# Kernel optimization log

Measured on AMD Instinct MI355X. Metric: run time of the kernel, lower is better.

Reference implementation:

```python
import jax, jax.numpy as jnp
import numpy as np

N_NODES = 25000
N_EDGES = 320000
IN_FEAT = 64
OUT_FEAT = 64
NUM_HEADS = 5
NUM_RELS = 20
NUM_BASES = 10


def setup_inputs() -> dict:
    key = jax.random.key(0)
    ks = jax.random.split(key, 8)
    feat = jax.random.normal(ks[0], (N_NODES, IN_FEAT), dtype=jnp.float32)
    src = jax.random.randint(ks[1], (N_EDGES,), 0, N_NODES, dtype=jnp.int64 if jax.config.jax_enable_x64 else jnp.int32)
    dst = jax.random.randint(ks[2], (N_EDGES,), 0, N_NODES, dtype=src.dtype)
    edge_type = jax.random.randint(ks[3], (N_EDGES,), 0, NUM_RELS, dtype=src.dtype)
    fc_w = jax.random.normal(ks[4], (IN_FEAT, OUT_FEAT), dtype=jnp.float32) * (2.0 / np.sqrt(IN_FEAT + OUT_FEAT))
    self_fc_w = jax.random.normal(ks[5], (IN_FEAT, NUM_HEADS * OUT_FEAT), dtype=jnp.float32) * (2.0 / np.sqrt(IN_FEAT + NUM_HEADS * OUT_FEAT))
    attention_weight = jax.random.normal(ks[6], (NUM_BASES, 2 * OUT_FEAT, NUM_HEADS), dtype=jnp.float32) * (2.0 / np.sqrt(2 * OUT_FEAT + NUM_HEADS))
    w_comp = jax.random.normal(ks[7], (NUM_RELS, NUM_BASES), dtype=jnp.float32) * (2.0 / np.sqrt(NUM_RELS + NUM_BASES))
    return {"feat": feat, "src": src, "dst": dst, "edge_type": edge_type,
            "fc_w": fc_w, "self_fc_w": self_fc_w,
            "attention_weight": attention_weight, "w_comp": w_comp}


def reference(feat, src, dst, edge_type, fc_w, self_fc_w, attention_weight, w_comp):
    # node projections
    z = feat @ fc_w                      # [N, F]
    self_z = feat @ self_fc_w            # [N, H*F]
    # basis-composed per-relation attention matrices: [R, 2F, H]
    attn_fcs = jnp.einsum('rb,bfh->rfh', w_comp, attention_weight)
    # per-edge attention: cat(src_z, dst_z) bmm gathered relation matrix
    z2 = jnp.concatenate([z[src], z[dst]], axis=1)          # [E, 2F]
    w_e = attn_fcs[edge_type]                                # [E, 2F, H] irregular gather
    att = jax.nn.leaky_relu(jnp.einsum('ef,efh->eh', z2, w_e), negative_slope=0.01)  # [E, H]
    # message = outer(att, src_z) flattened, segment-summed over dst
    msg = (att[:, :, None] * z[src][:, None, :]).reshape(att.shape[0], -1)  # [E, H*F]
    h = jax.ops.segment_sum(msg, dst, num_segments=feat.shape[0])            # [N, H*F]
    h = h + self_z  # self interaction; activation is None
    return h
```

## Files before the change

### kernel.cpp

```cpp
#include <hip/hip_runtime.h>
#include <hip/hip_bf16.h>

#define N_NODES 25000
#define N_EDGES 320000
#define F 64
#define H 5
#define R 20
#define B 10
#define HF 320
#define GEMMB 391
#define SCATB 625
#define MPAD 25024
#define CAP 64

typedef __attribute__((ext_vector_type(8))) short short8;
typedef __attribute__((ext_vector_type(4))) short short4v;
typedef __attribute__((ext_vector_type(4))) float float4v;

__device__ __forceinline__ float ldf(const void* p, int f32, int i) {
    if (f32) return ((const float*)p)[i];
    else     return __bfloat162float(((const __hip_bfloat16*)p)[i]);
}
__device__ __forceinline__ int ldi(const void* p, int i64, int i) {
    if (i64) return ((const int*)p)[2 * i];
    else     return ((const int*)p)[i];
}
__device__ __forceinline__ float b2f(unsigned short u) {
    union { unsigned u32; float f; } v; v.u32 = ((unsigned)u) << 16; return v.f;
}
__device__ __forceinline__ short f2bs(float x) {
    __hip_bfloat16 v = __float2bfloat16(x); return *(short*)&v;
}

__device__ __forceinline__ int probe_f32(const void* feat_raw) {
    unsigned w = ((const unsigned*)feat_raw)[threadIdx.x & 63];
    unsigned e = (w >> 7) & 0xFF;
    unsigned long long m = __ballot(e >= 110 && e <= 140);
    return __popcll(m) < 32;
}
__device__ __forceinline__ int probe_i64(const void* src_raw) {
    unsigned v = ((const unsigned*)src_raw)[2 * (threadIdx.x & 63) + 1];
    unsigned long long m = __ballot(v == 0);
    return __popcll(m) > 32;
}

__global__ void k0_setup(const void* __restrict__ feat,
                         const void* __restrict__ fcw, const void* __restrict__ sfw,
                         const void* __restrict__ aw, const void* __restrict__ wc,
                         __hip_bfloat16* __restrict__ Wpack,
                         __hip_bfloat16* __restrict__ W2pack,
                         int* __restrict__ cnt) {
    const int f32 = probe_f32(feat);
    const int idx = blockIdx.x * 256 + threadIdx.x;
    if (idx < N_NODES) cnt[idx] = 0;
    if (idx < 24576) {
        int j = idx & 7, lane = (idx >> 3) & 63, fq = idx >> 9;
        int q = fq & 1, t = fq >> 1;
        int k = (q ? 32 : 0) + ((lane >> 4) << 3) + j;
        int c = t * 16 + (lane & 15);
        float v = (c < HF) ? ldf(sfw, f32, k * HF + c) : ldf(fcw, f32, k * F + (c - HF));
        Wpack[idx] = __float2bfloat16(v);
    } else if (idx < 24576 + 20480) {
        int id2 = idx - 24576;
        int j = id2 & 7, lane = (id2 >> 3) & 63, fq = id2 >> 9;
        int q = fq & 1, t = fq >> 1;
        int k = (q ? 32 : 0) + ((lane >> 4) << 3) + j;
        int c = t * 16 + (lane & 15);
        int r = c >> 4, part = (c >> 3) & 1, h = c & 7;
        float acc = 0.f;
        if (h < H) {
#pragma unroll
            for (int bb = 0; bb < B; ++bb)
                acc += ldf(wc, f32, r * B + bb) *
                       ldf(aw, f32, bb * (2 * F * H) + (part * F + k) * H + h);
        }
        W2pack[id2] = __float2bfloat16(acc);
    }
}

__global__ __launch_bounds__(512) void k2_gemm(const void* __restrict__ feat,
                                               const void* __restrict__ srcp,
                                               const void* __restrict__ dstp,
                                               const void* __restrict__ etp,
                                               const __hip_bfloat16* __restrict__ Wpack,
                                               const __hip_bfloat16* __restrict__ W2pack,
                                               __hip_bfloat16* __restrict__ selfz,
                                               __hip_bfloat16* __restrict__ zc,
                                               __hip_bfloat16* __restrict__ a_src,
                                               __hip_bfloat16* __restrict__ a_dst,
                                               int* __restrict__ cnt,
                                               unsigned* __restrict__ perm) {
    __shared__ short zl[64][66];
    const int tid = threadIdx.x;

    if (blockIdx.x >= GEMMB) {
        const int i64 = probe_i64(srcp);
        const int e = (blockIdx.x - GEMMB) * 512 + tid;
        if (e < N_EDGES) {
            int d = ldi(dstp, i64, e);
            int s = ldi(srcp, i64, e);
            int r = ldi(etp, i64, e);
            int pos = atomicAdd(&cnt[d], 1);
            if (pos < CAP) perm[d * CAP + pos] = ((unsigned)r << 16) | (unsigned)s;
        }
        return;
    }

    const int f32 = probe_f32(feat);
    const int wave = tid >> 6, lane = tid & 63;
    const int quad = lane >> 4, col = lane & 15;
    const int wv = wave & 3, gh = wave >> 2;
    const int r0 = blockIdx.x * 64;

    short8 a0g[2], a1g[2];
#pragma unroll
    for (int gg = 0; gg < 2; ++gg) {
        const int g = gh * 2 + gg;
        int am = r0 + g * 16 + col;
        if (am >= N_NODES) am = N_NODES - 1;
        if (f32) {
            const float* Af = (const float*)feat;
            float4v f0 = *(const float4v*)(Af + am * F + quad * 8);
            float4v f1 = *(const float4v*)(Af + am * F + quad * 8 + 4);
            float4v g0 = *(const float4v*)(Af + am * F + 32 + quad * 8);
            float4v g1 = *(const float4v*)(Af + am * F + 32 + quad * 8 + 4);
#pragma unroll
            for (int j = 0; j < 4; ++j) {
                a0g[gg][j] = f2bs(f0[j]); a0g[gg][j + 4] = f2bs(f1[j]);
                a1g[gg][j] = f2bs(g0[j]); a1g[gg][j + 4] = f2bs(g1[j]);
            }
        } else {
            const __hip_bfloat16* A = (const __hip_bfloat16*)feat;
            a0g[gg] = *(const short8*)(A + am * F + quad * 8);
            a1g[gg] = *(const short8*)(A + am * F + 32 + quad * 8);
        }
    }

    const short8* Wp = (const short8*)Wpack;

    {
        const int t = 20 + wv;
        short8 b0 = Wp[(t * 2 + 0) * 64 + lane];
        short8 b1 = Wp[(t * 2 + 1) * 64 + lane];
        const int cb = wv * 16 + quad * 4;
#pragma unroll
        for (int gg = 0; gg < 2; ++gg) {
            const int g = gh * 2 + gg;
            float4v acc = {0.f, 0.f, 0.f, 0.f};
            acc = __builtin_amdgcn_mfma_f32_16x16x32_bf16(b0, a0g[gg], acc, 0, 0, 0);
            acc = __builtin_amdgcn_mfma_f32_16x16x32_bf16(b1, a1g[gg], acc, 0, 0, 0);
            short4v pv;
#pragma unroll
            for (int j = 0; j < 4; ++j) pv[j] = f2bs(acc[j]);
            const int row = r0 + g * 16 + col;
            *(short4v*)(zc + row * F + cb) = pv;
            *(short4v*)&zl[g * 16 + col][cb] = pv;
        }
    }
    __syncthreads();

    short8 c0g[2], c1g[2];
#pragma unroll
    for (int gg = 0; gg < 2; ++gg) {
        const int g = gh * 2 + gg;
        c0g[gg] = *(const short8*)&zl[g * 16 + col][quad * 8];
        c1g[gg] = *(const short8*)&zl[g * 16 + col][32 + quad * 8];
    }

#pragma unroll
    for (int tt = 0; tt < 5; ++tt) {
        const int t = wv * 5 + tt;
        short8 b0 = Wp[(t * 2 + 0) * 64 + lane];
        short8 b1 = Wp[(t * 2 + 1) * 64 + lane];
#pragma unroll
        for (int gg = 0; gg < 2; ++gg) {
            const int g = gh * 2 + gg;
            float4v acc = {0.f, 0.f, 0.f, 0.f};
            acc = __builtin_amdgcn_mfma_f32_16x16x32_bf16(b0, a0g[gg], acc, 0, 0, 0);
            acc = __builtin_amdgcn_mfma_f32_16x16x32_bf16(b1, a1g[gg], acc, 0, 0, 0);
            short4v pv;
#pragma unroll
            for (int j = 0; j < 4; ++j) pv[j] = f2bs(acc[j]);
            const int row = r0 + g * 16 + col;
            *(short4v*)(selfz + row * HF + t * 16 + quad * 4) = pv;
        }
    }

    const short8* W2p = (const short8*)W2pack;
    __hip_bfloat16* dsta = (quad & 2) ? a_dst : a_src;
    const int hoff = (quad & 1) * 4;
#pragma unroll
    for (int tt = 0; tt < 5; ++tt) {
        const int t = wv * 5 + tt;
        short8 b0 = W2p[(t * 2 + 0) * 64 + lane];
        short8 b1 = W2p[(t * 2 + 1) * 64 + lane];
#pragma unroll
        for (int gg = 0; gg < 2; ++gg) {
            const int g = gh * 2 + gg;
            float4v acc = {0.f, 0.f, 0.f, 0.f};
            acc = __builtin_amdgcn_mfma_f32_16x16x32_bf16(b0, c0g[gg], acc, 0, 0, 0);
            acc = __builtin_amdgcn_mfma_f32_16x16x32_bf16(b1, c1g[gg], acc, 0, 0, 0);
            short4v pv;
#pragma unroll
            for (int j = 0; j < 4; ++j) pv[j] = f2bs(acc[j]);
            const int row = r0 + g * 16 + col;
            *(short4v*)(dsta + row * 160 + t * 8 + hoff) = pv;
        }
    }
}

__global__ __launch_bounds__(256, 8) void k4_agg(const void* __restrict__ feat_raw,
                                                 const __hip_bfloat16* __restrict__ selfz,
                                                 const unsigned short* __restrict__ zc,
                                                 const __hip_bfloat16* __restrict__ a_src,
                                                 const __hip_bfloat16* __restrict__ a_dst,
                                                 const int* __restrict__ cnt,
                                                 const unsigned* __restrict__ perm,
                                                 void* __restrict__ out) {
    const int f32 = probe_f32(feat_raw);
    const int tid = threadIdx.x;
    const int wid = tid >> 6, lane = tid & 63;
    const int d = blockIdx.x * 4 + wid;

    const unsigned pk = perm[d * CAP + lane];
    int n = cnt[d];
    if (n > CAP) n = CAP;
    const int s_l = (int)(pk & 0xFFFFu), r_l = (int)(pk >> 16);

    const short* as = (const short*)a_src;
    const short* ad = (const short*)a_dst;

    float av0 = 0.f, av1 = 0.f, av2 = 0.f, av3 = 0.f, av4 = 0.f;
    if (lane < n) {
        short8 sv = *(const short8*)(as + s_l * 160 + r_l * 8);
        short8 dv = *(const short8*)(ad + d * 160 + r_l * 8);
        float t0 = b2f((unsigned short)sv[0]) + b2f((unsigned short)dv[0]);
        float t1 = b2f((unsigned short)sv[1]) + b2f((unsigned short)dv[1]);
        float t2 = b2f((unsigned short)sv[2]) + b2f((unsigned short)dv[2]);
        float t3 = b2f((unsigned short)sv[3]) + b2f((unsigned short)dv[3]);
        float t4 = b2f((unsigned short)sv[4]) + b2f((unsigned short)dv[4]);
        av0 = fmaxf(t0, 0.01f * t0);
        av1 = fmaxf(t1, 0.01f * t1);
        av2 = fmaxf(t2, 0.01f * t2);
        av3 = fmaxf(t3, 0.01f * t3);
        av4 = fmaxf(t4, 0.01f * t4);
    }

    float acc[H] = {0.f, 0.f, 0.f, 0.f, 0.f};
    int e = 0;
    for (; e + 4 <= n; e += 4) {
        int s_[4];
#pragma unroll
        for (int u = 0; u < 4; ++u) s_[u] = __shfl(s_l, e + u);
        float zs[4];
#pragma unroll
        for (int u = 0; u < 4; ++u) zs[u] = b2f(zc[s_[u] * F + lane]);
#pragma unroll
        for (int u = 0; u < 4; ++u) {
            acc[0] += __shfl(av0, e + u) * zs[u];
            acc[1] += __shfl(av1, e + u) * zs[u];
            acc[2] += __shfl(av2, e + u) * zs[u];
            acc[3] += __shfl(av3, e + u) * zs[u];
            acc[4] += __shfl(av4, e + u) * zs[u];
        }
    }
    for (; e < n; ++e) {
        int s = __shfl(s_l, e);
        float zs = b2f(zc[s * F + lane]);
        acc[0] += __shfl(av0, e) * zs;
        acc[1] += __shfl(av1, e) * zs;
        acc[2] += __shfl(av2, e) * zs;
        acc[3] += __shfl(av3, e) * zs;
        acc[4] += __shfl(av4, e) * zs;
    }

    const int ob = d * HF + lane;
    if (f32) {
        float* o = (float*)out;
#pragma unroll
        for (int h = 0; h < H; ++h)
            o[ob + h * F] = acc[h] + __bfloat162float(selfz[ob + h * F]);
    } else {
        __hip_bfloat16* o = (__hip_bfloat16*)out;
#pragma unroll
        for (int h = 0; h < H; ++h)
            o[ob + h * F] = __float2bfloat16(acc[h] + __bfloat162float(selfz[ob + h * F]));
    }
}

extern "C" void kernel_launch(void* const* d_in, const int* in_sizes, int n_in,
                              void* d_out, int out_size, void* d_ws, size_t ws_size,
                              hipStream_t stream) {
    const void* feat = d_in[0];
    const void* src  = d_in[1];
    const void* dst  = d_in[2];
    const void* et   = d_in[3];
    const void* fcw  = d_in[4];
    const void* sfw  = d_in[5];
    const void* aw   = d_in[6];
    const void* wc   = d_in[7];

    char* w = (char*)d_ws;
    __hip_bfloat16* selfz  = (__hip_bfloat16*)w;  w += (size_t)MPAD * HF * 2;
    __hip_bfloat16* zc     = (__hip_bfloat16*)w;  w += (size_t)MPAD * F * 2;
    __hip_bfloat16* a_src  = (__hip_bfloat16*)w;  w += (size_t)MPAD * 160 * 2;
    __hip_bfloat16* a_dst  = (__hip_bfloat16*)w;  w += (size_t)MPAD * 160 * 2;
    __hip_bfloat16* Wpack  = (__hip_bfloat16*)w;  w += 24576 * 2;
    __hip_bfloat16* W2pack = (__hip_bfloat16*)w;  w += 20480 * 2;
    unsigned* perm = (unsigned*)w;                w += (size_t)N_NODES * CAP * 4;
    int* cnt       = (int*)w;

    k0_setup<<<176, 256, 0, stream>>>(feat, fcw, sfw, aw, wc, Wpack, W2pack, cnt);
    k2_gemm<<<GEMMB + SCATB, 512, 0, stream>>>(feat, src, dst, et,
                                               Wpack, W2pack, selfz, zc,
                                               a_src, a_dst, cnt, perm);
    k4_agg<<<N_NODES / 4, 256, 0, stream>>>(feat, selfz, (const unsigned short*)zc,
                                            a_src, a_dst, cnt, perm, d_out);
}
```

Measured before the change: 141.4 us.

## Fold weight packing into GEMM kernel and replace setup kernel with memset

Removes the separate k0_setup kernel. Each GEMM wave now builds its bf16 MFMA B-fragments directly from the raw weight tensors, including the basis-composed attention weights, and cnt is cleared with hipMemsetAsync. This saves one kernel launch and the round trip of the packed weights through global memory. In exchange, all 391 GEMM blocks redo the strided weight loads and the 10-term basis sums, which adds latency and ALU work inside the GEMM.

```diff
diff --git a/kernel.cpp b/kernel.cpp
--- a/kernel.cpp
+++ b/kernel.cpp
@@ -44,46 +44,49 @@
     return __popcll(m) > 32;
 }
 
-__global__ void k0_setup(const void* __restrict__ feat,
-                         const void* __restrict__ fcw, const void* __restrict__ sfw,
-                         const void* __restrict__ aw, const void* __restrict__ wc,
-                         __hip_bfloat16* __restrict__ Wpack,
-                         __hip_bfloat16* __restrict__ W2pack,
-                         int* __restrict__ cnt) {
-    const int f32 = probe_f32(feat);
-    const int idx = blockIdx.x * 256 + threadIdx.x;
-    if (idx < N_NODES) cnt[idx] = 0;
-    if (idx < 24576) {
-        int j = idx & 7, lane = (idx >> 3) & 63, fq = idx >> 9;
-        int q = fq & 1, t = fq >> 1;
-        int k = (q ? 32 : 0) + ((lane >> 4) << 3) + j;
-        int c = t * 16 + (lane & 15);
-        float v = (c < HF) ? ldf(sfw, f32, k * HF + c) : ldf(fcw, f32, k * F + (c - HF));
-        Wpack[idx] = __float2bfloat16(v);
-    } else if (idx < 24576 + 20480) {
-        int id2 = idx - 24576;
-        int j = id2 & 7, lane = (id2 >> 3) & 63, fq = id2 >> 9;
-        int q = fq & 1, t = fq >> 1;
-        int k = (q ? 32 : 0) + ((lane >> 4) << 3) + j;
-        int c = t * 16 + (lane & 15);
-        int r = c >> 4, part = (c >> 3) & 1, h = c & 7;
+__device__ __forceinline__ short8 packW(const void* sfw, const void* fcw,
+                                        int f32, int t, int q, int lane) {
+    short8 w;
+    const int col = lane & 15;
+    const int kb = (q ? 32 : 0) + ((lane >> 4) << 3);
+#pragma unroll
+    for (int j = 0; j < 8; ++j) {
+        const int k = kb + j;
+        float v = (t < 20) ? ldf(sfw, f32, k * HF + t * 16 + col)
+                           : ldf(fcw, f32, k * F + (t - 20) * 16 + col);
+        w[j] = f2bs(v);
+    }
+    return w;
+}
+__device__ __forceinline__ short8 packW2(const void* aw, const void* wc,
+                                         int f32, int t, int q, int lane) {
+    short8 w;
+    const int col = lane & 15;
+    const int part = (col >> 3) & 1, h = col & 7;
+    const int kb = (q ? 32 : 0) + ((lane >> 4) << 3);
+#pragma unroll
+    for (int j = 0; j < 8; ++j) {
+        const int k = kb + j;
         float acc = 0.f;
         if (h < H) {
 #pragma unroll
             for (int bb = 0; bb < B; ++bb)
-                acc += ldf(wc, f32, r * B + bb) *
+                acc += ldf(wc, f32, t * B + bb) *
                        ldf(aw, f32, bb * (2 * F * H) + (part * F + k) * H + h);
         }
-        W2pack[id2] = __float2bfloat16(acc);
-    }
+        w[j] = f2bs(acc);
+    }
+    return w;
 }
 
 __global__ __launch_bounds__(512) void k2_gemm(const void* __restrict__ feat,
                                                const void* __restrict__ srcp,
                                                const void* __restrict__ dstp,
                                                const void* __restrict__ etp,
-                                               const __hip_bfloat16* __restrict__ Wpack,
-                                               const __hip_bfloat16* __restrict__ W2pack,
+                                               const void* __restrict__ fcw,
+                                               const void* __restrict__ sfw,
+                                               const void* __restrict__ aw,
+                                               const void* __restrict__ wc,
                                                __hip_bfloat16* __restrict__ selfz,
                                                __hip_bfloat16* __restrict__ zc,
                                                __hip_bfloat16* __restrict__ a_src,
@@ -136,12 +139,10 @@
         }
     }
 
-    const short8* Wp = (const short8*)Wpack;
-
     {
         const int t = 20 + wv;
-        short8 b0 = Wp[(t * 2 + 0) * 64 + lane];
-        short8 b1 = Wp[(t * 2 + 1) * 64 + lane];
+        short8 b0 = packW(sfw, fcw, f32, t, 0, lane);
+        short8 b1 = packW(sfw, fcw, f32, t, 1, lane);
         const int cb = wv * 16 + quad * 4;
 #pragma unroll
         for (int gg = 0; gg < 2; ++gg) {
@@ -170,8 +171,8 @@
 #pragma unroll
     for (int tt = 0; tt < 5; ++tt) {
         const int t = wv * 5 + tt;
-        short8 b0 = Wp[(t * 2 + 0) * 64 + lane];
-        short8 b1 = Wp[(t * 2 + 1) * 64 + lane];
+        short8 b0 = packW(sfw, fcw, f32, t, 0, lane);
+        short8 b1 = packW(sfw, fcw, f32, t, 1, lane);
 #pragma unroll
         for (int gg = 0; gg < 2; ++gg) {
             const int g = gh * 2 + gg;
@@ -186,14 +187,13 @@
         }
     }
 
-    const short8* W2p = (const short8*)W2pack;
     __hip_bfloat16* dsta = (quad & 2) ? a_dst : a_src;
     const int hoff = (quad & 1) * 4;
 #pragma unroll
     for (int tt = 0; tt < 5; ++tt) {
         const int t = wv * 5 + tt;
-        short8 b0 = W2p[(t * 2 + 0) * 64 + lane];
-        short8 b1 = W2p[(t * 2 + 1) * 64 + lane];
+        short8 b0 = packW2(aw, wc, f32, t, 0, lane);
+        short8 b1 = packW2(aw, wc, f32, t, 1, lane);
 #pragma unroll
         for (int gg = 0; gg < 2; ++gg) {
             const int g = gh * 2 + gg;
@@ -305,15 +305,12 @@
     __hip_bfloat16* zc     = (__hip_bfloat16*)w;  w += (size_t)MPAD * F * 2;
     __hip_bfloat16* a_src  = (__hip_bfloat16*)w;  w += (size_t)MPAD * 160 * 2;
     __hip_bfloat16* a_dst  = (__hip_bfloat16*)w;  w += (size_t)MPAD * 160 * 2;
-    __hip_bfloat16* Wpack  = (__hip_bfloat16*)w;  w += 24576 * 2;
-    __hip_bfloat16* W2pack = (__hip_bfloat16*)w;  w += 20480 * 2;
     unsigned* perm = (unsigned*)w;                w += (size_t)N_NODES * CAP * 4;
     int* cnt       = (int*)w;
 
-    k0_setup<<<176, 256, 0, stream>>>(feat, fcw, sfw, aw, wc, Wpack, W2pack, cnt);
-    k2_gemm<<<GEMMB + SCATB, 512, 0, stream>>>(feat, src, dst, et,
-                                               Wpack, W2pack, selfz, zc,
-                                               a_src, a_dst, cnt, perm);
+    hipMemsetAsync(cnt, 0, (size_t)N_NODES * 4, stream);
+    k2_gemm<<<GEMMB + SCATB, 512, 0, stream>>>(feat, src, dst, et, fcw, sfw, aw, wc,
+                                               selfz, zc, a_src, a_dst, cnt, perm);
     k4_agg<<<N_NODES / 4, 256, 0, stream>>>(feat, selfz, (const unsigned short*)zc,
                                             a_src, a_dst, cnt, perm, d_out);
 }
```

New measurement: 263.8 us. 1.87x slower.
